# Kernel tuning notes

Measured on AMD Instinct MI355X. Metric: run time of the kernel, lower is better.

Reference implementation:

```python
import jax, jax.numpy as jnp
import numpy as np

B = 256
DIN = 63
D1 = DIN + 1            # 64, after appending ones column
F = D1 ** 3             # 262144 kronecker features
H1, H2 = 256, 128
EPS = 1e-5
NEG_SLOPE = 0.1


def setup_inputs() -> dict:
    key = jax.random.key(0)
    ks = jax.random.split(key, 8)
    vec1 = jax.random.normal(ks[0], (B, DIN), dtype=jnp.float32)
    vec2 = jax.random.normal(ks[1], (B, DIN), dtype=jnp.float32)
    vec3 = jax.random.normal(ks[2], (B, DIN), dtype=jnp.float32)
    W1 = jax.random.normal(ks[3], (F, H1), dtype=jnp.float32) * (1.0 / np.sqrt(F))
    b1 = jnp.zeros((H1,), jnp.float32)
    g1 = jnp.ones((H1,), jnp.float32)
    beta1 = jnp.zeros((H1,), jnp.float32)
    rm1 = jnp.zeros((H1,), jnp.float32)
    rv1 = jnp.ones((H1,), jnp.float32)
    W2 = jax.random.normal(ks[4], (H1, H2), dtype=jnp.float32) * (1.0 / np.sqrt(H1))
    b2 = jnp.zeros((H2,), jnp.float32)
    g2 = jnp.ones((H2,), jnp.float32)
    beta2 = jnp.zeros((H2,), jnp.float32)
    rm2 = jnp.zeros((H2,), jnp.float32)
    rv2 = jnp.ones((H2,), jnp.float32)
    Wc = jax.random.normal(ks[5], (H2, 1), dtype=jnp.float32) * (1.0 / np.sqrt(H2))
    bc = jnp.zeros((1,), jnp.float32)
    return dict(vec1=vec1, vec2=vec2, vec3=vec3,
                W1=W1, b1=b1, g1=g1, beta1=beta1, rm1=rm1, rv1=rv1,
                W2=W2, b2=b2, g2=g2, beta2=beta2, rm2=rm2, rv2=rv2,
                Wc=Wc, bc=bc)


def _leaky(x):
    return jnp.where(x >= 0, x, NEG_SLOPE * x)


def _bn_eval(x, gamma, beta, rmean, rvar):
    return (x - rmean) * jax.lax.rsqrt(rvar + EPS) * gamma + beta


def reference(vec1, vec2, vec3, W1, b1, g1, beta1, rm1, rv1,
              W2, b2, g2, beta2, rm2, rv2, Wc, bc):
    ones = jnp.ones((vec1.shape[0], 1), vec1.dtype)
    v1 = jnp.concatenate([vec1, ones], axis=1)  # [B, D1]
    v2 = jnp.concatenate([vec2, ones], axis=1)
    v3 = jnp.concatenate([vec3, ones], axis=1)
    # x12[b, i*D1+j] = v1[b,i]*v2[b,j]; x[b, (i*D1+j)*D1+k] = x12*v3[b,k]
    x = jnp.einsum('bi,bj,bk->bijk', v1, v2, v3).reshape(v1.shape[0], -1)  # [B, F]
    h = _leaky(x @ W1 + b1)
    h = _bn_eval(h, g1, beta1, rm1, rv1)  # dropout is identity in eval
    h = _leaky(h @ W2 + b2)
    h = _bn_eval(h, g2, beta2, rm2, rv2)
    return h @ Wc + bc  # [B, 1]
```

## Files before the change

### kernel.cpp

```cpp
#include <hip/hip_runtime.h>
#include <stdint.h>

#define DIN   63
#define BATCH 256
#define H1    256
#define H2    128
#define NEG   0.1f
#define EPSB  1e-5f

typedef _Float16 half2_t __attribute__((ext_vector_type(2)));
typedef _Float16 half8_t __attribute__((ext_vector_type(8)));
typedef float   float4_t __attribute__((ext_vector_type(4)));

#define V12_STRIDE 66
#define WT_STRIDE  72
#define WT_BUF     (32 * WT_STRIDE)

union AFrag { half8_t v; half2_t h2[4]; };

static __device__ inline half2_t pack_f16(float a, float b) {
    half2_t h; h.x = (_Float16)a; h.y = (_Float16)b; return h;
}

__global__ __launch_bounds__(256, 2)
void gemm1_kernel(const float* __restrict__ vec1, const float* __restrict__ vec2,
                  const float* __restrict__ vec3, const float* __restrict__ W1,
                  float* __restrict__ partial)
{
    const int nt    = blockIdx.x;
    const int islab = blockIdx.y;
    const int n0    = nt * 32;
    const int tid   = threadIdx.x;
    const int lane  = tid & 63;
    const int wm    = tid >> 6;
    const int m16   = lane & 15;
    const int quad  = lane >> 4;

    __shared__ __align__(16) _Float16 v12all[BATCH * V12_STRIDE];
    __shared__ __align__(16) _Float16 Wt[2 * WT_BUF];

    {
        const int b = tid;
        const float v1v = (islab < DIN) ? vec1[b * DIN + islab] : 1.0f;
        #pragma unroll
        for (int jp = 0; jp < 32; ++jp) {
            const int j0 = 2 * jp;
            const float a0 = v1v * ((j0     < DIN) ? vec2[b * DIN + j0    ] : 1.0f);
            const float a1 = v1v * ((j0 + 1 < DIN) ? vec2[b * DIN + j0 + 1] : 1.0f);
            *reinterpret_cast<half2_t*>(&v12all[b * V12_STRIDE + j0]) = pack_f16(a0, a1);
        }
    }

    half2_t v3h[4][2][4];
    #pragma unroll
    for (int Mt = 0; Mt < 4; ++Mt) {
        const int b = wm * 64 + Mt * 16 + m16;
        #pragma unroll
        for (int kk = 0; kk < 2; ++kk) {
            const int kb = kk * 32 + quad * 8;
            float v[8];
            #pragma unroll
            for (int t = 0; t < 8; ++t) {
                const int k = kb + t;
                v[t] = (k < DIN) ? vec3[b * DIN + k] : 1.0f;
            }
            #pragma unroll
            for (int s = 0; s < 4; ++s)
                v3h[Mt][kk][s] = pack_f16(v[2 * s], v[2 * s + 1]);
        }
    }

    const int kp  = tid & 31;
    const int nch = tid >> 5;

    float4_t sa, sb;
    {
        const size_t f = (size_t)islab * 4096 + 2 * kp;
        const float* p0 = W1 + f * H1 + n0 + nch * 4;
        sa = *reinterpret_cast<const float4_t*>(p0);
        sb = *reinterpret_cast<const float4_t*>(p0 + H1);
    }
    {
        _Float16* wb = &Wt[0];
        #pragma unroll
        for (int s = 0; s < 4; ++s)
            *reinterpret_cast<half2_t*>(&wb[(nch * 4 + s) * WT_STRIDE + 2 * kp]) =
                pack_f16(sa[s], sb[s]);
    }
    __syncthreads();

    float4_t acc[4][2];
    #pragma unroll
    for (int Mt = 0; Mt < 4; ++Mt)
        #pragma unroll
        for (int Nt = 0; Nt < 2; ++Nt)
            acc[Mt][Nt] = (float4_t){0.f, 0.f, 0.f, 0.f};

    for (int j = 0; j < 64; ++j) {
        const int cur = j & 1;
        if (j + 1 < 64) {
            const size_t f = (size_t)islab * 4096 + (size_t)(j + 1) * 64 + 2 * kp;
            const float* p0 = W1 + f * H1 + n0 + nch * 4;
            sa = *reinterpret_cast<const float4_t*>(p0);
            sb = *reinterpret_cast<const float4_t*>(p0 + H1);
        }

        const _Float16* wb = &Wt[cur * WT_BUF];
        half8_t bfrag[2][2];
        #pragma unroll
        for (int kk = 0; kk < 2; ++kk)
            #pragma unroll
            for (int Nt = 0; Nt < 2; ++Nt) {
                const int n = Nt * 16 + m16;
                bfrag[kk][Nt] = *reinterpret_cast<const half8_t*>(
                    &wb[n * WT_STRIDE + kk * 32 + quad * 8]);
            }

        #pragma unroll
        for (int Mt = 0; Mt < 4; ++Mt) {
            const int b = wm * 64 + Mt * 16 + m16;
            const _Float16 v12 = v12all[b * V12_STRIDE + j];
            half2_t vv; vv.x = v12; vv.y = v12;
            #pragma unroll
            for (int kk = 0; kk < 2; ++kk) {
                AFrag af;
                #pragma unroll
                for (int s = 0; s < 4; ++s) af.h2[s] = vv * v3h[Mt][kk][s];
                acc[Mt][0] = __builtin_amdgcn_mfma_f32_16x16x32_f16(af.v, bfrag[kk][0], acc[Mt][0], 0, 0, 0);
                acc[Mt][1] = __builtin_amdgcn_mfma_f32_16x16x32_f16(af.v, bfrag[kk][1], acc[Mt][1], 0, 0, 0);
            }
        }
        __syncthreads();
        if (j + 1 < 64) {
            _Float16* wb2 = &Wt[(cur ^ 1) * WT_BUF];
            #pragma unroll
            for (int s = 0; s < 4; ++s)
                *reinterpret_cast<half2_t*>(&wb2[(nch * 4 + s) * WT_STRIDE + 2 * kp]) =
                    pack_f16(sa[s], sb[s]);
        }
        __syncthreads();
    }

    #pragma unroll
    for (int Mt = 0; Mt < 4; ++Mt) {
        const int brow = wm * 64 + Mt * 16 + quad * 4;
        #pragma unroll
        for (int Nt = 0; Nt < 2; ++Nt) {
            const int n = n0 + Nt * 16 + m16;
            #pragma unroll
            for (int r = 0; r < 4; ++r)
                partial[(size_t)islab * (BATCH * H1) + (size_t)(brow + r) * H1 + n] = acc[Mt][Nt][r];
        }
    }
}

__global__ __launch_bounds__(256)
void tail_kernel(const float* __restrict__ partial,
                 const float* __restrict__ b1, const float* __restrict__ g1,
                 const float* __restrict__ be1, const float* __restrict__ rm1,
                 const float* __restrict__ rv1,
                 const float* __restrict__ W2, const float* __restrict__ b2,
                 const float* __restrict__ g2, const float* __restrict__ be2,
                 const float* __restrict__ rm2, const float* __restrict__ rv2,
                 const float* __restrict__ Wc, const float* __restrict__ bc,
                 float* __restrict__ out)
{
    const int b = blockIdx.x;
    const int t = threadIdx.x;
    __shared__ float h1row[H1];
    __shared__ float ph[2][H2];
    __shared__ float h2row[H2];

    float s = 0.0f;
    const float* p = partial + (size_t)b * H1 + t;
    #pragma unroll 8
    for (int i = 0; i < 64; ++i) s += p[(size_t)i * (BATCH * H1)];
    s += b1[t];
    s = (s >= 0.0f) ? s : NEG * s;
    s = (s - rm1[t]) * rsqrtf(rv1[t] + EPSB) * g1[t] + be1[t];
    h1row[t] = s;
    __syncthreads();

    {
        const int n    = t & 127;
        const int half = t >> 7;
        const int h0   = half * 128;
        float acc = 0.0f;
        #pragma unroll 4
        for (int h = 0; h < 128; ++h)
            acc += h1row[h0 + h] * W2[(size_t)(h0 + h) * H2 + n];
        ph[half][n] = acc;
    }
    __syncthreads();
    if (t < H2) {
        float acc = ph[0][t] + ph[1][t] + b2[t];
        acc = (acc >= 0.0f) ? acc : NEG * acc;
        acc = (acc - rm2[t]) * rsqrtf(rv2[t] + EPSB) * g2[t] + be2[t];
        h2row[t] = acc;
    }
    __syncthreads();
    if (t < 64) {
        float v = h2row[t] * Wc[t] + h2row[t + 64] * Wc[t + 64];
        #pragma unroll
        for (int off = 32; off > 0; off >>= 1) v += __shfl_down(v, off);
        if (t == 0) out[b] = v + bc[0];
    }
}

extern "C" void kernel_launch(void* const* d_in, const int* in_sizes, int n_in,
                              void* d_out, int out_size, void* d_ws, size_t ws_size,
                              hipStream_t stream)
{
    const float* vec1 = (const float*)d_in[0];
    const float* vec2 = (const float*)d_in[1];
    const float* vec3 = (const float*)d_in[2];
    const float* W1   = (const float*)d_in[3];
    const float* b1   = (const float*)d_in[4];
    const float* g1   = (const float*)d_in[5];
    const float* be1  = (const float*)d_in[6];
    const float* rm1  = (const float*)d_in[7];
    const float* rv1  = (const float*)d_in[8];
    const float* W2   = (const float*)d_in[9];
    const float* b2   = (const float*)d_in[10];
    const float* g2   = (const float*)d_in[11];
    const float* be2  = (const float*)d_in[12];
    const float* rm2  = (const float*)d_in[13];
    const float* rv2  = (const float*)d_in[14];
    const float* Wc   = (const float*)d_in[15];
    const float* bc   = (const float*)d_in[16];

    float* partial = (float*)d_ws;

    gemm1_kernel<<<dim3(8, 64), 256, 0, stream>>>(vec1, vec2, vec3, W1, partial);
    tail_kernel<<<256, 256, 0, stream>>>(partial, b1, g1, be1, rm1, rv1,
                                         W2, b2, g2, be2, rm2, rv2, Wc, bc,
                                         (float*)d_out);
}
```

Baseline: 419.6 us.

## Stage two j-steps of W1 per barrier with a three-deep register prefetch

The GEMM1 main loop now handles 128 K-rows (two j values) per shared-memory stage instead of 64, which halves the number of iterations and cuts the barriers from two per step to one. W1 tiles are prefetched two stages ahead in alternating register sets and written into the other shared buffer before the barrier, so global load latency overlaps with MFMA work. The load pattern changes to 4-row by 4-column blocks stored as half4 into a wider transposed tile. The cost is more registers for the prefetched tiles and the doubled B fragments, which may lower occupancy.

```diff
diff --git a/kernel.cpp b/kernel.cpp
--- a/kernel.cpp
+++ b/kernel.cpp
@@ -9,16 +9,17 @@
 #define EPSB  1e-5f
 
 typedef _Float16 half2_t __attribute__((ext_vector_type(2)));
+typedef _Float16 half4_t __attribute__((ext_vector_type(4)));
 typedef _Float16 half8_t __attribute__((ext_vector_type(8)));
 typedef float   float4_t __attribute__((ext_vector_type(4)));
 
 #define V12_STRIDE 66
-#define WT_STRIDE  72
-#define WT_BUF     (32 * WT_STRIDE)
+#define WTS        136
+#define WT_BUF     (32 * WTS)
 
 union AFrag { half8_t v; half2_t h2[4]; };
 
-static __device__ inline half2_t pack_f16(float a, float b) {
+static __device__ __forceinline__ half2_t pack_f16(float a, float b) {
     half2_t h; h.x = (_Float16)a; h.y = (_Float16)b; return h;
 }
 
@@ -39,6 +40,22 @@
     __shared__ __align__(16) _Float16 v12all[BATCH * V12_STRIDE];
     __shared__ __align__(16) _Float16 Wt[2 * WT_BUF];
 
+    const int rr = (tid >> 3) * 4;
+    const int cl = (tid & 7) * 4;
+    const float* wload_base = W1 + ((size_t)islab * 4096 + rr) * H1 + n0 + cl;
+
+    float4_t t0[4], pA[4], pB[4];
+    {
+        #pragma unroll
+        for (int r = 0; r < 4; ++r) t0[r] = *(const float4_t*)(wload_base + (size_t)r * H1);
+        const float* p1 = wload_base + (size_t)128 * H1;
+        #pragma unroll
+        for (int r = 0; r < 4; ++r) pA[r] = *(const float4_t*)(p1 + (size_t)r * H1);
+        const float* p2 = wload_base + (size_t)256 * H1;
+        #pragma unroll
+        for (int r = 0; r < 4; ++r) pB[r] = *(const float4_t*)(p2 + (size_t)r * H1);
+    }
+
     {
         const int b = tid;
         const float v1v = (islab < DIN) ? vec1[b * DIN + islab] : 1.0f;
@@ -65,28 +82,22 @@
                 v[t] = (k < DIN) ? vec3[b * DIN + k] : 1.0f;
             }
             #pragma unroll
-            for (int s = 0; s < 4; ++s)
-                v3h[Mt][kk][s] = pack_f16(v[2 * s], v[2 * s + 1]);
-        }
-    }
-
-    const int kp  = tid & 31;
-    const int nch = tid >> 5;
-
-    float4_t sa, sb;
-    {
-        const size_t f = (size_t)islab * 4096 + 2 * kp;
-        const float* p0 = W1 + f * H1 + n0 + nch * 4;
-        sa = *reinterpret_cast<const float4_t*>(p0);
-        sb = *reinterpret_cast<const float4_t*>(p0 + H1);
-    }
-    {
-        _Float16* wb = &Wt[0];
-        #pragma unroll
-        for (int s = 0; s < 4; ++s)
-            *reinterpret_cast<half2_t*>(&wb[(nch * 4 + s) * WT_STRIDE + 2 * kp]) =
-                pack_f16(sa[s], sb[s]);
-    }
+            for (int s = 0; s < 4; ++s) v3h[Mt][kk][s] = pack_f16(v[2 * s], v[2 * s + 1]);
+        }
+    }
+
+    auto write_step = [&](int buf, const float4_t (&v)[4]) {
+        _Float16* wn = &Wt[buf * WT_BUF];
+        #pragma unroll
+        for (int sc = 0; sc < 4; ++sc) {
+            half4_t h;
+            h.x = (_Float16)v[0][sc]; h.y = (_Float16)v[1][sc];
+            h.z = (_Float16)v[2][sc]; h.w = (_Float16)v[3][sc];
+            *reinterpret_cast<half4_t*>(&wn[(cl + sc) * WTS + rr]) = h;
+        }
+    };
+
+    write_step(0, t0);
     __syncthreads();
 
     float4_t acc[4][2];
@@ -96,49 +107,54 @@
         for (int Nt = 0; Nt < 2; ++Nt)
             acc[Mt][Nt] = (float4_t){0.f, 0.f, 0.f, 0.f};
 
-    for (int j = 0; j < 64; ++j) {
-        const int cur = j & 1;
-        if (j + 1 < 64) {
-            const size_t f = (size_t)islab * 4096 + (size_t)(j + 1) * 64 + 2 * kp;
-            const float* p0 = W1 + f * H1 + n0 + nch * 4;
-            sa = *reinterpret_cast<const float4_t*>(p0);
-            sb = *reinterpret_cast<const float4_t*>(p0 + H1);
-        }
-
+    auto iter = [&](int s, float4_t (&pend)[4]) {
+        const int cur = s & 1;
         const _Float16* wb = &Wt[cur * WT_BUF];
-        half8_t bfrag[2][2];
-        #pragma unroll
-        for (int kk = 0; kk < 2; ++kk)
-            #pragma unroll
-            for (int Nt = 0; Nt < 2; ++Nt) {
-                const int n = Nt * 16 + m16;
-                bfrag[kk][Nt] = *reinterpret_cast<const half8_t*>(
-                    &wb[n * WT_STRIDE + kk * 32 + quad * 8]);
+
+        half8_t bfrag[2][2][2];
+        #pragma unroll
+        for (int jj = 0; jj < 2; ++jj)
+            #pragma unroll
+            for (int kk = 0; kk < 2; ++kk)
+                #pragma unroll
+                for (int Nt = 0; Nt < 2; ++Nt)
+                    bfrag[jj][kk][Nt] = *reinterpret_cast<const half8_t*>(
+                        &wb[(Nt * 16 + m16) * WTS + jj * 64 + kk * 32 + quad * 8]);
+
+        half2_t vj[4];
+        #pragma unroll
+        for (int Mt = 0; Mt < 4; ++Mt)
+            vj[Mt] = *reinterpret_cast<const half2_t*>(
+                &v12all[(wm * 64 + Mt * 16 + m16) * V12_STRIDE + 2 * s]);
+
+        if (s < 31) write_step(cur ^ 1, pend);
+        if (s < 29) {
+            const float* p = wload_base + (size_t)(s + 3) * 128 * H1;
+            #pragma unroll
+            for (int r = 0; r < 4; ++r) pend[r] = *(const float4_t*)(p + (size_t)r * H1);
+        }
+        __syncthreads();
+
+        #pragma unroll
+        for (int jj = 0; jj < 2; ++jj)
+            #pragma unroll
+            for (int Mt = 0; Mt < 4; ++Mt) {
+                half2_t vv; vv.x = vj[Mt][jj]; vv.y = vj[Mt][jj];
+                #pragma unroll
+                for (int kk = 0; kk < 2; ++kk) {
+                    AFrag af;
+                    #pragma unroll
+                    for (int sc = 0; sc < 4; ++sc) af.h2[sc] = vv * v3h[Mt][kk][sc];
+                    acc[Mt][0] = __builtin_amdgcn_mfma_f32_16x16x32_f16(af.v, bfrag[jj][kk][0], acc[Mt][0], 0, 0, 0);
+                    acc[Mt][1] = __builtin_amdgcn_mfma_f32_16x16x32_f16(af.v, bfrag[jj][kk][1], acc[Mt][1], 0, 0, 0);
+                }
             }
-
-        #pragma unroll
-        for (int Mt = 0; Mt < 4; ++Mt) {
-            const int b = wm * 64 + Mt * 16 + m16;
-            const _Float16 v12 = v12all[b * V12_STRIDE + j];
-            half2_t vv; vv.x = v12; vv.y = v12;
-            #pragma unroll
-            for (int kk = 0; kk < 2; ++kk) {
-                AFrag af;
-                #pragma unroll
-                for (int s = 0; s < 4; ++s) af.h2[s] = vv * v3h[Mt][kk][s];
-                acc[Mt][0] = __builtin_amdgcn_mfma_f32_16x16x32_f16(af.v, bfrag[kk][0], acc[Mt][0], 0, 0, 0);
-                acc[Mt][1] = __builtin_amdgcn_mfma_f32_16x16x32_f16(af.v, bfrag[kk][1], acc[Mt][1], 0, 0, 0);
-            }
-        }
-        __syncthreads();
-        if (j + 1 < 64) {
-            _Float16* wb2 = &Wt[(cur ^ 1) * WT_BUF];
-            #pragma unroll
-            for (int s = 0; s < 4; ++s)
-                *reinterpret_cast<half2_t*>(&wb2[(nch * 4 + s) * WT_STRIDE + 2 * kp]) =
-                    pack_f16(sa[s], sb[s]);
-        }
-        __syncthreads();
+    };
+
+    #pragma unroll 1
+    for (int s2 = 0; s2 < 32; s2 += 2) {
+        iter(s2,     pA);
+        iter(s2 + 1, pB);
     }
 
     #pragma unroll
```

Result: no change. 421.0 us (+0.3%).
